# Kernel tuning notes

Hardware: AMD Instinct MI355X
Metric: run time of the kernel (lower is better)

## Reference

```python
import jax, jax.numpy as jnp
import numpy as np

B, T, D, H = 64, 1024, 1024, 1024


def setup_inputs() -> dict:
    key = jax.random.key(0)
    k = jax.random.split(key, 5)
    s = 1.0 / np.sqrt(H)  # torch RNNCell init: U(-1/sqrt(H), 1/sqrt(H))
    return {
        "x": jax.random.normal(k[0], (B, T, D), jnp.float32),
        "W_ih": jax.random.uniform(k[1], (H, D), jnp.float32, -s, s),
        "W_hh": jax.random.uniform(k[2], (H, H), jnp.float32, -s, s),
        "b_ih": jax.random.uniform(k[3], (H,), jnp.float32, -s, s),
        "b_hh": jax.random.uniform(k[4], (H,), jnp.float32, -s, s),
    }


def reference(x, W_ih, W_hh, b_ih, b_hh):
    # DelayLineRNN2xOS with a tanh RNNCell:
    #   for i in range(T//2):
    #     h_eve = cell(x[:, 2i],   h_eve); states[:, 2i]   = h_eve
    #     h_odd = cell(x[:, 2i-1], h_odd); states[:, 2i-1] = h_odd   (note 2*0-1 == -1)
    Bn, Tn, _ = x.shape
    Hn = W_hh.shape[0]
    half = Tn // 2

    idx_eve = jnp.arange(half) * 2          # 0, 2, ..., T-2
    idx_odd = (idx_eve - 1) % Tn            # T-1, 1, 3, ..., T-3  (Python neg-index at i=0)

    # Precompute input projections for all timesteps (both biases folded in).
    gi = jnp.einsum('btd,hd->bth', x, W_ih) + b_ih + b_hh  # [B, T, H]
    ge = gi[:, idx_eve].transpose(1, 0, 2)                  # [half, B, H]
    go = gi[:, idx_odd].transpose(1, 0, 2)                  # [half, B, H]

    h0 = jnp.zeros((Bn, Hn), x.dtype)

    def step(carry, inp):
        he, ho = carry
        a, b = inp
        he = jnp.tanh(a + he @ W_hh.T)
        ho = jnp.tanh(b + ho @ W_hh.T)
        return (he, ho), (he, ho)

    (he_f, ho_f), (eve_s, odd_s) = jax.lax.scan(step, (h0, h0), (ge, go))

    # eve_s[i] -> slot 2i ; odd_s[i] -> slot (2i-1) mod T, i.e. sorted odd slots
    # [1, 3, ..., T-1] receive odd_s rolled left by one.
    odd_sorted = jnp.roll(odd_s, -1, axis=0)                # [half, B, H]
    states = jnp.stack([eve_s, odd_sorted], axis=1)         # [half, 2, B, H]
    states = states.reshape(Tn, Bn, Hn).transpose(1, 0, 2)  # [B, T, H]

    return states, he_f[None]  # (states, h_final[1, B, H])
```

## Files before the change

kernel.cpp:

```cpp
#include <hip/hip_runtime.h>

#define B_    64
#define T_    1024
#define H_    1024
#define HALF_ 512
#define NWG_SCAN 128
#define HBUF_HALF 131072

typedef short bf16x8 __attribute__((ext_vector_type(8)));
typedef short bf16x4 __attribute__((ext_vector_type(4)));
typedef _Float16 f16x8 __attribute__((ext_vector_type(8)));
typedef float f32x4  __attribute__((ext_vector_type(4)));
typedef unsigned int u32x4 __attribute__((ext_vector_type(4)));
typedef unsigned int u32x2 __attribute__((ext_vector_type(2)));

__device__ __forceinline__ short f2h(float f) {
    return (short)__builtin_bit_cast(unsigned short, (_Float16)f);
}

__device__ __forceinline__ bf16x4 pk4(f32x4 v) {
    unsigned w0, w1;
    asm("v_cvt_pk_bf16_f32 %0, %1, %2" : "=v"(w0) : "v"(v.x), "v"(v.y));
    asm("v_cvt_pk_bf16_f32 %0, %1, %2" : "=v"(w1) : "v"(v.z), "v"(v.w));
    u32x2 r; r[0] = w0; r[1] = w1;
    return __builtin_bit_cast(bf16x4, r);
}

__device__ __forceinline__ float tanh_fast(float x) {
    return 1.0f - 2.0f / (__expf(2.0f * x) + 1.0f);
}

#define BAR() do { \
    __builtin_amdgcn_sched_barrier(0); \
    asm volatile("s_waitcnt lgkmcnt(0)" ::: "memory"); \
    __builtin_amdgcn_sched_barrier(0); \
    __builtin_amdgcn_s_barrier(); \
    __builtin_amdgcn_sched_barrier(0); \
} while (0)

__global__ __launch_bounds__(256) void gi_gemm(
        const float* __restrict__ X, const float* __restrict__ Wih,
        const float* __restrict__ bih, const float* __restrict__ bhh,
        float* __restrict__ out) {
    __shared__ short As[128][40];
    __shared__ short Bs[128][40];
    const int bid = blockIdx.x;
    const int tn = bid & 7;
    const int tm = bid >> 3;
    const int tid = threadIdx.x;
    const int l  = tid & 63;
    const int w  = tid >> 6;
    const int wr = w >> 1, wc = w & 1;
    const int lc = l & 15,  lr = l >> 4;

    const float* Ab = X   + (size_t)tm * 128 * 1024;
    const float* Bb = Wih + (size_t)tn * 128 * 1024;
    const int srow = tid >> 3;
    const int sc4  = (tid & 7) * 4;

    f32x4 acc[4][4];
#pragma unroll
    for (int m = 0; m < 4; m++)
#pragma unroll
        for (int n = 0; n < 4; n++) acc[m][n] = (f32x4){0.f, 0.f, 0.f, 0.f};

    f32x4 ra[4], rb[4];
#pragma unroll
    for (int c = 0; c < 4; c++) {
        ra[c] = *reinterpret_cast<const f32x4*>(Ab + (size_t)(srow + 32*c) * 1024 + sc4);
        rb[c] = *reinterpret_cast<const f32x4*>(Bb + (size_t)(srow + 32*c) * 1024 + sc4);
    }

    for (int k0 = 0; k0 < 1024; k0 += 32) {
        __syncthreads();
#pragma unroll
        for (int c = 0; c < 4; c++) {
            *reinterpret_cast<bf16x4*>(&As[srow + 32*c][sc4]) = pk4(ra[c]);
            *reinterpret_cast<bf16x4*>(&Bs[srow + 32*c][sc4]) = pk4(rb[c]);
        }
        __syncthreads();
        if (k0 + 32 < 1024) {
            const float* Ak = Ab + k0 + 32;
            const float* Bk = Bb + k0 + 32;
#pragma unroll
            for (int c = 0; c < 4; c++) {
                ra[c] = *reinterpret_cast<const f32x4*>(Ak + (size_t)(srow + 32*c) * 1024 + sc4);
                rb[c] = *reinterpret_cast<const f32x4*>(Bk + (size_t)(srow + 32*c) * 1024 + sc4);
            }
        }
        bf16x8 af[4], bfr[4];
#pragma unroll
        for (int m = 0; m < 4; m++)
            af[m] = *reinterpret_cast<bf16x8*>(&As[wr*64 + m*16 + lc][lr*8]);
#pragma unroll
        for (int n = 0; n < 4; n++)
            bfr[n] = *reinterpret_cast<bf16x8*>(&Bs[wc*64 + n*16 + lc][lr*8]);
#pragma unroll
        for (int m = 0; m < 4; m++)
#pragma unroll
            for (int n = 0; n < 4; n++)
                acc[m][n] = __builtin_amdgcn_mfma_f32_16x16x32_bf16(af[m], bfr[n], acc[m][n], 0, 0, 0);
    }

#pragma unroll
    for (int n = 0; n < 4; n++) {
        const int col = tn*128 + wc*64 + n*16 + lc;
        const float bs = bih[col] + bhh[col];
#pragma unroll
        for (int m = 0; m < 4; m++) {
            const int row0 = tm*128 + wr*64 + m*16 + lr*4;
#pragma unroll
            for (int j = 0; j < 4; j++)
                out[(size_t)(row0 + j) * 1024 + col] = acc[m][n][j] + bs;
        }
    }
}

__global__ __launch_bounds__(256, 1) void rnn_scan(
        const float* __restrict__ Whh, float* __restrict__ out,
        short* __restrict__ hbuf) {
    __shared__ short hB[16 * 1024];
    __shared__ float giS[16 * 68];
    __shared__ float htrF[16 * 68];
    const int wg = blockIdx.x;
    const int p  = wg >> 6;
    const int g  = (wg >> 4) & 3;
    const int s  = wg & 15;
    const int tid = threadIdx.x;
    const int l  = tid & 63;
    const int w  = tid >> 6;
    const int lc = l & 15, lr = l >> 4;
    const int sb = tid >> 4;
    const int sg = tid & 15;

    bf16x8 breg[32];
    {
        const float* wrow = Whh + (size_t)(s*64 + w*16 + lc) * 1024;
#pragma unroll
        for (int kc = 0; kc < 32; kc++) {
            f32x4 v0 = *reinterpret_cast<const f32x4*>(wrow + kc*32 + lr*8);
            f32x4 v1 = *reinterpret_cast<const f32x4*>(wrow + kc*32 + lr*8 + 4);
            bf16x8 q = { f2h(v0.x), f2h(v0.y), f2h(v0.z), f2h(v0.w),
                         f2h(v1.x), f2h(v1.y), f2h(v1.z), f2h(v1.w) };
            breg[kc] = q;
        }
    }

    const unsigned grp_base = (unsigned)((p*64 + g*16) * 1024);
    const unsigned hst_off = grp_base + (unsigned)(s*1024 + w*256 + lr*64 + lc*4);
    const int lcol = w*16 + lr*4;

    int dly = 8;

    for (int step = 0; step < HALF_; step++) {
        const int tt = (p == 0) ? (2*step) : (step == 0 ? T_-1 : 2*step - 1);
        const int epw = step % 3 + 1;
        const int epv = (step + 2) % 3 + 1;
        f32x4 acc = (f32x4){0.f, 0.f, 0.f, 0.f};
        f32x4 giv;
        const float* ga = out + (size_t)(((g*16 + sb) * T_ + tt) * H_ + s*64 + sg*4);

        if (step) {
            for (int i = 0; i < dly; i++)
                asm volatile("s_sleep 1" ::: "memory");
            bf16x8 hl[8];
            const short* hc = hbuf + (size_t)((step+1) & 1) * HBUF_HALF
                            + grp_base + (unsigned)(tid*8);
#pragma unroll
            for (int c = 0; c < 8; c++)
                asm volatile("global_load_dwordx4 %0, %1, off sc0 sc1"
                             : "=v"(hl[c]) : "v"(hc + c*2048) : "memory");
            asm volatile("global_load_dwordx4 %0, %1, off"
                         : "=v"(giv) : "v"(ga) : "memory");
            const unsigned pat = (unsigned)((epv & 1) | (((epv >> 1) & 1) << 16));
            unsigned pend = 0;
            asm volatile("s_waitcnt vmcnt(1)" ::: "memory");
            __builtin_amdgcn_sched_barrier(0);
#pragma unroll
            for (int c = 0; c < 8; c++) {
                u32x4 d = __builtin_bit_cast(u32x4, hl[c]);
                unsigned m = ((d[0] & 0x00010001u) ^ pat) | ((d[1] & 0x00010001u) ^ pat)
                           | ((d[2] & 0x00010001u) ^ pat) | ((d[3] & 0x00010001u) ^ pat);
                if (!__all(m == 0)) pend |= 1u << c;
            }
            const int hadRetry = (pend != 0);
            while (pend) {
#pragma unroll
                for (int c = 0; c < 8; c++)
                    if (pend & (1u << c))
                        asm volatile("global_load_dwordx4 %0, %1, off sc0 sc1"
                                     : "=v"(hl[c]) : "v"(hc + c*2048) : "memory");
                asm volatile("s_waitcnt vmcnt(0)" ::: "memory");
                __builtin_amdgcn_sched_barrier(0);
#pragma unroll
                for (int c = 0; c < 8; c++) {
                    if (pend & (1u << c)) {
                        u32x4 d = __builtin_bit_cast(u32x4, hl[c]);
                        unsigned m = ((d[0] & 0x00010001u) ^ pat) | ((d[1] & 0x00010001u) ^ pat)
                                   | ((d[2] & 0x00010001u) ^ pat) | ((d[3] & 0x00010001u) ^ pat);
                        if (__all(m == 0)) pend &= ~(1u << c);
                    }
                }
            }
            dly = hadRetry ? (dly > 44 ? 48 : dly + 4) : (dly ? dly - 1 : 0);
            asm volatile("s_waitcnt vmcnt(0)" ::: "memory");
            __builtin_amdgcn_sched_barrier(0);
            *reinterpret_cast<f32x4*>(&giS[sb*68 + sg*4]) = giv;
#pragma unroll
            for (int c = 0; c < 8; c++) {
                bf16x4 lo = { hl[c][0], hl[c][1], hl[c][2], hl[c][3] };
                bf16x4 hi = { hl[c][4], hl[c][5], hl[c][6], hl[c][7] };
                const int gidx0 = c*512 + tid*2;
                const int b0 = gidx0 & 15;
                const int g8 = gidx0 >> 4;
                *reinterpret_cast<bf16x4*>(&hB[b0*1024 + ((g8 ^ b0) << 2)]) = lo;
                *reinterpret_cast<bf16x4*>(&hB[(b0+1)*1024 + ((g8 ^ (b0+1)) << 2)]) = hi;
            }
            BAR();
            f32x4 a0 = (f32x4){0,0,0,0}, a1 = (f32x4){0,0,0,0};
            f32x4 a2 = (f32x4){0,0,0,0}, a3 = (f32x4){0,0,0,0};
#pragma unroll
            for (int kc = 0; kc < 32; kc += 4) {
#pragma unroll
                for (int q = 0; q < 4; q++) {
                    const int k8 = (kc + q) * 8 + lr * 2;
                    bf16x4 lo = *reinterpret_cast<const bf16x4*>(&hB[lc*1024 + (((k8    ) ^ lc) << 2)]);
                    bf16x4 hi = *reinterpret_cast<const bf16x4*>(&hB[lc*1024 + (((k8 + 1) ^ lc) << 2)]);
                    bf16x8 hf = { lo[0], lo[1], lo[2], lo[3], hi[0], hi[1], hi[2], hi[3] };
                    f32x4& aq = (q == 0) ? a0 : (q == 1) ? a1 : (q == 2) ? a2 : a3;
                    aq = __builtin_amdgcn_mfma_f32_16x16x32_f16(
                        __builtin_bit_cast(f16x8, breg[kc + q]),
                        __builtin_bit_cast(f16x8, hf), aq, 0, 0, 0);
                }
            }
            acc = (a0 + a1) + (a2 + a3);
        } else {
            asm volatile("global_load_dwordx4 %0, %1, off"
                         : "=v"(giv) : "v"(ga) : "memory");
            asm volatile("s_waitcnt vmcnt(0)" ::: "memory");
            __builtin_amdgcn_sched_barrier(0);
            *reinterpret_cast<f32x4*>(&giS[sb*68 + sg*4]) = giv;
            BAR();
        }

        f32x4 gi4 = *reinterpret_cast<f32x4*>(&giS[lc*68 + lcol]);

        float hv0 = tanh_fast(acc[0] + gi4[0]);
        float hv1 = tanh_fast(acc[1] + gi4[1]);
        float hv2 = tanh_fast(acc[2] + gi4[2]);
        float hv3 = tanh_fast(acc[3] + gi4[3]);
        const unsigned e0 = (unsigned)(epw & 1);
        const unsigned e1 = (unsigned)((epw >> 1) & 1);
        unsigned u0 = ((unsigned)__builtin_bit_cast(unsigned short, (_Float16)hv0) & 0xFFFEu) | e0;
        unsigned u1 = ((unsigned)__builtin_bit_cast(unsigned short, (_Float16)hv1) & 0xFFFEu) | e1;
        unsigned u2 = ((unsigned)__builtin_bit_cast(unsigned short, (_Float16)hv2) & 0xFFFEu) | e0;
        unsigned u3 = ((unsigned)__builtin_bit_cast(unsigned short, (_Float16)hv3) & 0xFFFEu) | e1;
        u32x2 pk; pk[0] = u0 | (u1 << 16); pk[1] = u2 | (u3 << 16);

        if (step < HALF_ - 1) {
            short* hn = hbuf + (size_t)(step & 1) * HBUF_HALF + hst_off;
            asm volatile("global_store_dwordx2 %0, %1, off sc0 sc1"
                         :: "v"(hn), "v"(pk) : "memory");
        }

        {
            f32x4 hv; hv[0] = hv0; hv[1] = hv1; hv[2] = hv2; hv[3] = hv3;
            *reinterpret_cast<f32x4*>(&htrF[lc*68 + lcol]) = hv;
        }
        BAR();
        {
            f32x4 ov = *reinterpret_cast<f32x4*>(&htrF[sb*68 + sg*4]);
            float* op_ = out + (size_t)(((g*16 + sb) * T_ + tt) * H_ + s*64 + sg*4);
            asm volatile("global_store_dwordx4 %0, %1, off"
                         :: "v"(op_), "v"(ov) : "memory");
            if (p == 0 && step == HALF_ - 1) {
                float* fp_ = out + (size_t)B_*T_*H_ + (size_t)((g*16 + sb) * H_ + s*64 + sg*4);
                asm volatile("global_store_dwordx4 %0, %1, off"
                             :: "v"(fp_), "v"(ov) : "memory");
            }
        }
    }
}

extern "C" void kernel_launch(void* const* d_in, const int* in_sizes, int n_in,
                              void* d_out, int out_size, void* d_ws, size_t ws_size,
                              hipStream_t stream) {
    const float* X   = (const float*)d_in[0];
    const float* Wih = (const float*)d_in[1];
    const float* Whh = (const float*)d_in[2];
    const float* bih = (const float*)d_in[3];
    const float* bhh = (const float*)d_in[4];
    float* out = (float*)d_out;

    short* hbuf = (short*)d_ws;

    hipMemsetAsync(hbuf, 0, (size_t)2 * HBUF_HALF * 2, stream);
    gi_gemm<<<dim3(4096), dim3(256), 0, stream>>>(X, Wih, bih, bhh, out);
    rnn_scan<<<dim3(NWG_SCAN), dim3(256), 0, stream>>>(Whh, out, hbuf);
}
```

Measured before the change: 1.790 ms.

## Double-buffer LDS staging to drop per-step output barrier in RNN scan

Doubles the shared-memory buffers for hidden state, gate inputs and the output transpose, indexed by step parity. Each step's transposed output store is deferred to the next step, where it is read after that step's existing barrier. This removes one workgroup barrier from every step of the 512-step serial recurrence, shortening the critical path. It costs double the LDS footprint and adds a final barrier and store after the loop.

```diff
diff --git a/kernel.cpp b/kernel.cpp
--- a/kernel.cpp
+++ b/kernel.cpp
@@ -119,9 +119,9 @@
 __global__ __launch_bounds__(256, 1) void rnn_scan(
         const float* __restrict__ Whh, float* __restrict__ out,
         short* __restrict__ hbuf) {
-    __shared__ short hB[16 * 1024];
-    __shared__ float giS[16 * 68];
-    __shared__ float htrF[16 * 68];
+    __shared__ short hB[2][16 * 1024];
+    __shared__ float giS[2][16 * 68];
+    __shared__ float htrF[2][16 * 68];
     const int wg = blockIdx.x;
     const int p  = wg >> 6;
     const int g  = (wg >> 4) & 3;
@@ -151,14 +151,16 @@
     const int lcol = w*16 + lr*4;
 
     int dly = 8;
+    float* prev_op = nullptr;
 
     for (int step = 0; step < HALF_; step++) {
         const int tt = (p == 0) ? (2*step) : (step == 0 ? T_-1 : 2*step - 1);
         const int epw = step % 3 + 1;
         const int epv = (step + 2) % 3 + 1;
+        const int buf = step & 1;
         f32x4 acc = (f32x4){0.f, 0.f, 0.f, 0.f};
         f32x4 giv;
-        const float* ga = out + (size_t)(((g*16 + sb) * T_ + tt) * H_ + s*64 + sg*4);
+        float* ga = out + (size_t)(((g*16 + sb) * T_ + tt) * H_ + s*64 + sg*4);
 
         if (step) {
             for (int i = 0; i < dly; i++)
@@ -205,7 +207,7 @@
             dly = hadRetry ? (dly > 44 ? 48 : dly + 4) : (dly ? dly - 1 : 0);
             asm volatile("s_waitcnt vmcnt(0)" ::: "memory");
             __builtin_amdgcn_sched_barrier(0);
-            *reinterpret_cast<f32x4*>(&giS[sb*68 + sg*4]) = giv;
+            *reinterpret_cast<f32x4*>(&giS[buf][sb*68 + sg*4]) = giv;
 #pragma unroll
             for (int c = 0; c < 8; c++) {
                 bf16x4 lo = { hl[c][0], hl[c][1], hl[c][2], hl[c][3] };
@@ -213,8 +215,8 @@
                 const int gidx0 = c*512 + tid*2;
                 const int b0 = gidx0 & 15;
                 const int g8 = gidx0 >> 4;
-                *reinterpret_cast<bf16x4*>(&hB[b0*1024 + ((g8 ^ b0) << 2)]) = lo;
-                *reinterpret_cast<bf16x4*>(&hB[(b0+1)*1024 + ((g8 ^ (b0+1)) << 2)]) = hi;
+                *reinterpret_cast<bf16x4*>(&hB[buf][b0*1024 + ((g8 ^ b0) << 2)]) = lo;
+                *reinterpret_cast<bf16x4*>(&hB[buf][(b0+1)*1024 + ((g8 ^ (b0+1)) << 2)]) = hi;
             }
             BAR();
             f32x4 a0 = (f32x4){0,0,0,0}, a1 = (f32x4){0,0,0,0};
@@ -224,8 +226,8 @@
 #pragma unroll
                 for (int q = 0; q < 4; q++) {
                     const int k8 = (kc + q) * 8 + lr * 2;
-                    bf16x4 lo = *reinterpret_cast<const bf16x4*>(&hB[lc*1024 + (((k8    ) ^ lc) << 2)]);
-                    bf16x4 hi = *reinterpret_cast<const bf16x4*>(&hB[lc*1024 + (((k8 + 1) ^ lc) << 2)]);
+                    bf16x4 lo = *reinterpret_cast<const bf16x4*>(&hB[buf][lc*1024 + (((k8    ) ^ lc) << 2)]);
+                    bf16x4 hi = *reinterpret_cast<const bf16x4*>(&hB[buf][lc*1024 + (((k8 + 1) ^ lc) << 2)]);
                     bf16x8 hf = { lo[0], lo[1], lo[2], lo[3], hi[0], hi[1], hi[2], hi[3] };
                     f32x4& aq = (q == 0) ? a0 : (q == 1) ? a1 : (q == 2) ? a2 : a3;
                     aq = __builtin_amdgcn_mfma_f32_16x16x32_f16(
@@ -239,11 +241,11 @@
                          : "=v"(giv) : "v"(ga) : "memory");
             asm volatile("s_waitcnt vmcnt(0)" ::: "memory");
             __builtin_amdgcn_sched_barrier(0);
-            *reinterpret_cast<f32x4*>(&giS[sb*68 + sg*4]) = giv;
+            *reinterpret_cast<f32x4*>(&giS[buf][sb*68 + sg*4]) = giv;
             BAR();
         }
 
-        f32x4 gi4 = *reinterpret_cast<f32x4*>(&giS[lc*68 + lcol]);
+        f32x4 gi4 = *reinterpret_cast<f32x4*>(&giS[buf][lc*68 + lcol]);
 
         float hv0 = tanh_fast(acc[0] + gi4[0]);
         float hv1 = tanh_fast(acc[1] + gi4[1]);
@@ -265,19 +267,25 @@
 
         {
             f32x4 hv; hv[0] = hv0; hv[1] = hv1; hv[2] = hv2; hv[3] = hv3;
-            *reinterpret_cast<f32x4*>(&htrF[lc*68 + lcol]) = hv;
-        }
-        BAR();
-        {
-            f32x4 ov = *reinterpret_cast<f32x4*>(&htrF[sb*68 + sg*4]);
-            float* op_ = out + (size_t)(((g*16 + sb) * T_ + tt) * H_ + s*64 + sg*4);
+            *reinterpret_cast<f32x4*>(&htrF[buf][lc*68 + lcol]) = hv;
+        }
+        if (step) {
+            f32x4 ov = *reinterpret_cast<f32x4*>(&htrF[buf ^ 1][sb*68 + sg*4]);
             asm volatile("global_store_dwordx4 %0, %1, off"
-                         :: "v"(op_), "v"(ov) : "memory");
-            if (p == 0 && step == HALF_ - 1) {
-                float* fp_ = out + (size_t)B_*T_*H_ + (size_t)((g*16 + sb) * H_ + s*64 + sg*4);
-                asm volatile("global_store_dwordx4 %0, %1, off"
-                             :: "v"(fp_), "v"(ov) : "memory");
-            }
+                         :: "v"(prev_op), "v"(ov) : "memory");
+        }
+        prev_op = ga;
+    }
+
+    BAR();
+    {
+        f32x4 ov = *reinterpret_cast<f32x4*>(&htrF[(HALF_ - 1) & 1][sb*68 + sg*4]);
+        asm volatile("global_store_dwordx4 %0, %1, off"
+                     :: "v"(prev_op), "v"(ov) : "memory");
+        if (p == 0) {
+            float* fp_ = out + (size_t)B_*T_*H_ + (size_t)((g*16 + sb) * H_ + s*64 + sg*4);
+            asm volatile("global_store_dwordx4 %0, %1, off"
+                         :: "v"(fp_), "v"(ov) : "memory");
         }
     }
 }
```

Result: slower. 1.834 ms (+2.5%).
